# Kernel tuning notes

Measured on AMD Instinct MI355X. Metric: run time of the kernel, lower is better.

The kernel has to match this reference:

```python
import jax, jax.numpy as jnp
import numpy as np

B, D, T, H, CHUNK, MAX_REL = 4, 512, 8192, 8, 64, 2
HD = D // H


def setup_inputs() -> dict:
    key = jax.random.key(0)
    ks = jax.random.split(key, 16)
    s = 0.02
    inp = {
        "q": jax.random.normal(ks[0], (B, D, T), jnp.float32),
        "k": jax.random.normal(ks[1], (B, D, T), jnp.float32),
        "v": jax.random.normal(ks[2], (B, D, T), jnp.float32),
        "masks": jnp.ones((B, 1, T), jnp.float32),
        "Wq": jax.random.normal(ks[3], (D, D), jnp.float32) * s,
        "bq": jnp.zeros((D,), jnp.float32),
        "Wk": jax.random.normal(ks[4], (D, D), jnp.float32) * s,
        "bk": jnp.zeros((D,), jnp.float32),
        "Wv": jax.random.normal(ks[5], (D, D), jnp.float32) * s,
        "bv": jnp.zeros((D,), jnp.float32),
        "Wo": jax.random.normal(ks[6], (D, D), jnp.float32) * s,
        "bo": jnp.zeros((D,), jnp.float32),
        "rel_k": jax.random.normal(ks[7], (2 * MAX_REL + 1, HD), jnp.float32) * s,
        "rel_v": jax.random.normal(ks[8], (2 * MAX_REL + 1, HD), jnp.float32) * s,
    }
    return inp


def reference(q, k, v, masks, Wq, bq, Wk, bk, Wv, bv, Wo, bo, rel_k, rel_v):
    n = CHUNK
    g = T // n  # T is a multiple of chunck_size -> no padding branch
    bg = B * g

    # (B, D, T) -> (B, T, D) -> (B*g, n, D) chunking
    qt = jnp.swapaxes(q, 1, 2).reshape(bg, n, D)
    kt = jnp.swapaxes(k, 1, 2).reshape(bg, n, D)
    vt = jnp.swapaxes(v, 1, 2).reshape(bg, n, D)
    cm = jnp.swapaxes(masks, 1, 2).reshape(bg, n)  # per-chunk mask values

    # gen_key_padding_mask: chunks that are entirely zero are un-masked (set to 1)
    all_zero = jnp.sum(cm, axis=-1) == 0.0
    cm_fixed = jnp.where(all_zero[:, None], 1.0, cm)
    kpm = cm_fixed == 0.0  # (bg, n) True = masked key

    # projections (torch Linear: x @ W.T + b)
    qp = qt @ Wq.T + bq
    kp = kt @ Wk.T + bk
    vp = vt @ Wv.T + bv

    qh = qp.reshape(bg, n, H, HD).transpose(0, 2, 1, 3)  # (bg, H, n, hd)
    kh = kp.reshape(bg, n, H, HD).transpose(0, 2, 1, 3)
    vh = vp.reshape(bg, n, H, HD).transpose(0, 2, 1, 3)

    # content-content scores
    attn1 = jnp.einsum('bhqd,bhkd->bhqk', qh, kh)

    # relative position indices: clip(k - q, -max, max) + max
    ridx = jnp.clip(jnp.arange(n)[None, :] - jnp.arange(n)[:, None], -MAX_REL, MAX_REL) + MAX_REL
    rk = rel_k[ridx]  # (n, n, hd)
    rv = rel_v[ridx]  # (n, n, hd)

    # content-position scores
    attn2 = jnp.einsum('bhqd,qkd->bhqk', qh, rk)

    scale = jnp.sqrt(jnp.asarray(HD, jnp.float32))
    attn = (attn1 + attn2) / scale
    attn = jnp.where(kpm[:, None, None, :], -jnp.inf, attn)
    p = jax.nn.softmax(attn, axis=-1)  # (bg, H, n, n)

    w1 = jnp.einsum('bhqk,bhkd->bhqd', p, vh)
    w2 = jnp.einsum('bhqk,qkd->bhqd', p, rv)
    xo = (w1 + w2).transpose(0, 2, 1, 3).reshape(bg, n, D)
    xo = xo @ Wo.T + bo

    out = xo.reshape(B, T, D)
    out = jnp.swapaxes(out, 1, 2)  # (B, D, T)
    return out * masks
```

## Files before the change

### kernel.cpp

```cpp
#include <hip/hip_runtime.h>


typedef __attribute__((ext_vector_type(8))) short short8;
typedef __attribute__((ext_vector_type(4))) float f32x4;
typedef __attribute__((ext_vector_type(2))) unsigned int uint2v;
typedef __attribute__((ext_vector_type(4))) unsigned short ushort4v;

#define DEV static __device__ __forceinline__

DEV unsigned short f2bf(float f) {
  union { float f; unsigned int u; } x; x.f = f;
  unsigned int r = x.u + 0x7fffu + ((x.u >> 16) & 1u);
  return (unsigned short)(r >> 16);
}
DEV float bf2f(unsigned short h) {
  union { unsigned int u; float f; } x; x.u = ((unsigned int)h) << 16;
  return x.f;
}

constexpr int Bn = 4, Dm = 512, Tn = 8192, NC = 64;
constexpr int Gn = Tn / NC;
constexpr int BG = Bn * Gn;
constexpr int WSZ = Dm * Dm;

__global__ void wcvt_kernel(const float* __restrict__ wq, const float* __restrict__ wk,
                            const float* __restrict__ wv, const float* __restrict__ wo,
                            unsigned short* __restrict__ dst) {
  int i = (blockIdx.x * blockDim.x + threadIdx.x) * 4;
  const float* src = (i < WSZ) ? wq : (i < 2 * WSZ) ? wk : (i < 3 * WSZ) ? wv : wo;
  int off = i & (WSZ - 1);
  f32x4 v = *(const f32x4*)(src + off);
  ushort4v o;
  o[0] = f2bf(v[0]); o[1] = f2bf(v[1]); o[2] = f2bf(v[2]); o[3] = f2bf(v[3]);
  *(ushort4v*)(dst + i) = o;
}

__global__ __launch_bounds__(512, 2)
void fused_kernel(const float* __restrict__ qx, const float* __restrict__ kx,
                  const float* __restrict__ vx, const float* __restrict__ masks,
                  const unsigned short* __restrict__ wbf,
                  const float* __restrict__ bq, const float* __restrict__ bk,
                  const float* __restrict__ bv, const float* __restrict__ bo,
                  const float* __restrict__ relk, const float* __restrict__ relv,
                  float* __restrict__ out)
{
  extern __shared__ char lds[];
  const int tid  = threadIdx.x;
  const int lane = tid & 63;
  const int w    = tid >> 6;
  const int l15  = lane & 15;
  const int lg   = lane >> 4;
  const int c    = blockIdx.x;
  const int b    = c >> 7;
  const int t0   = (c & (Gn - 1)) * NC;

  char* xbuf = lds;
  char* regA = lds + 16 * 1024 + w * 16 * 1024;
  char* regB = regA + 8 * 1024;

  float cmv = masks[(size_t)b * Tn + t0 + lane];
  unsigned long long nzb = __ballot(cmv != 0.0f);
  unsigned long long kpm = (nzb == 0ull) ? 0ull : __ballot(cmv == 0.0f);

  const f32x4 fzero = {0.f, 0.f, 0.f, 0.f};

  auto project = [&](const float* __restrict__ xin, const unsigned short* __restrict__ Wp,
                     f32x4 (&acc)[4][4]) {
#pragma unroll
    for (int mi = 0; mi < 4; ++mi)
#pragma unroll
      for (int ni = 0; ni < 4; ++ni) acc[mi][ni] = fzero;
    const size_t xbase = (size_t)b * Dm * Tn + t0 + lane;
    for (int s = 0; s < 4; ++s) {
      const int d0 = s * 128;
      short8 xs[2];
#pragma unroll
      for (int cc = 0; cc < 2; ++cc)
#pragma unroll
        for (int j = 0; j < 8; ++j) {
          float f = xin[xbase + (size_t)(d0 + 16 * w + 8 * cc + j) * Tn];
          xs[cc][j] = (short)f2bf(f);
        }
      short8 wf[4][4];
#pragma unroll
      for (int ni = 0; ni < 4; ++ni)
#pragma unroll
        for (int kk = 0; kk < 4; ++kk) {
          int o = 64 * w + ni * 16 + l15;
          int d = d0 + kk * 32 + lg * 8;
          wf[ni][kk] = *(const short8*)(Wp + o * Dm + d);
        }
      __syncthreads();
#pragma unroll
      for (int cc = 0; cc < 2; ++cc) {
        int off = (lane * 256 + (16 * w + 8 * cc) * 2) ^ ((lane & 15) << 4);
        *(short8*)(xbuf + off) = xs[cc];
      }
      __syncthreads();
#pragma unroll
      for (int kk = 0; kk < 4; ++kk) {
        short8 af[4];
#pragma unroll
        for (int mi = 0; mi < 4; ++mi) {
          int t = mi * 16 + l15;
          int off = (t * 256 + (kk * 32 + lg * 8) * 2) ^ ((t & 15) << 4);
          af[mi] = *(const short8*)(xbuf + off);
        }
#pragma unroll
        for (int ni = 0; ni < 4; ++ni)
#pragma unroll
          for (int mi = 0; mi < 4; ++mi)
            acc[mi][ni] = __builtin_amdgcn_mfma_f32_16x16x32_bf16(af[mi], wf[ni][kk],
                                                                  acc[mi][ni], 0, 0, 0);
      }
    }
  };

  f32x4 acc[4][4];

  project(qx, wbf + 0 * WSZ, acc);
#pragma unroll
  for (int ni = 0; ni < 4; ++ni) {
    float bia = bq[64 * w + ni * 16 + l15];
    int hd = ni * 16 + l15;
#pragma unroll
    for (int mi = 0; mi < 4; ++mi)
#pragma unroll
      for (int rr = 0; rr < 4; ++rr) {
        int t = mi * 16 + lg * 4 + rr;
        int off = (t * 128 + hd * 2) ^ ((t & 7) << 4);
        *(unsigned short*)(regA + off) = f2bf(acc[mi][ni][rr] + bia);
      }
  }

  project(kx, wbf + 1 * WSZ, acc);
#pragma unroll
  for (int ni = 0; ni < 4; ++ni) {
    float bia = bk[64 * w + ni * 16 + l15];
    int hd = ni * 16 + l15;
#pragma unroll
    for (int mi = 0; mi < 4; ++mi)
#pragma unroll
      for (int rr = 0; rr < 4; ++rr) {
        int t = mi * 16 + lg * 4 + rr;
        int off = (t * 128 + hd * 2) ^ ((t & 7) << 4);
        *(unsigned short*)(regB + off) = f2bf(acc[mi][ni][rr] + bia);
      }
  }

  f32x4 sacc[4][4];
#pragma unroll
  for (int mi = 0; mi < 4; ++mi)
#pragma unroll
    for (int ni = 0; ni < 4; ++ni) sacc[mi][ni] = fzero;
#pragma unroll
  for (int kk = 0; kk < 2; ++kk) {
    short8 aq[4], bkf[4];
#pragma unroll
    for (int mi = 0; mi < 4; ++mi) {
      int t = mi * 16 + l15;
      int off = (t * 128 + (kk * 32 + lg * 8) * 2) ^ ((t & 7) << 4);
      aq[mi]  = *(const short8*)(regA + off);
      bkf[mi] = *(const short8*)(regB + off);
    }
#pragma unroll
    for (int ni = 0; ni < 4; ++ni)
#pragma unroll
      for (int mi = 0; mi < 4; ++mi)
        sacc[mi][ni] = __builtin_amdgcn_mfma_f32_16x16x32_bf16(aq[mi], bkf[ni],
                                                               sacc[mi][ni], 0, 0, 0);
  }

  float qr0 = 0, qr1 = 0, qr2 = 0, qr3 = 0, qr4 = 0;
#pragma unroll
  for (int g = 0; g < 8; ++g) {
    short8 q8 = *(const short8*)(regA + ((lane * 128 + g * 16) ^ ((lane & 7) << 4)));
#pragma unroll
    for (int j = 0; j < 8; ++j) {
      float qf = bf2f((unsigned short)q8[j]);
      qr0 += qf * relk[0 * 64 + g * 8 + j];
      qr1 += qf * relk[1 * 64 + g * 8 + j];
      qr2 += qf * relk[2 * 64 + g * 8 + j];
      qr3 += qf * relk[3 * 64 + g * 8 + j];
      qr4 += qf * relk[4 * 64 + g * 8 + j];
    }
  }

  const float scale = 0.125f;
#pragma unroll
  for (int mi = 0; mi < 4; ++mi)
#pragma unroll
    for (int rr = 0; rr < 4; ++rr) {
      int qt = mi * 16 + lg * 4 + rr;
      float q0 = __shfl(qr0, qt), q1 = __shfl(qr1, qt), q2 = __shfl(qr2, qt),
            q3 = __shfl(qr3, qt), q4 = __shfl(qr4, qt);
      float sv[4];
#pragma unroll
      for (int ni = 0; ni < 4; ++ni) {
        int kt = ni * 16 + l15;
        int dd = kt - qt;
        float a2 = (dd <= -2) ? q0 : (dd == -1) ? q1 : (dd == 0) ? q2 : (dd == 1) ? q3 : q4;
        float s = (sacc[mi][ni][rr] + a2) * scale;
        if ((kpm >> kt) & 1ull) s = -1e30f;
        sv[ni] = s;
      }
      float m = fmaxf(fmaxf(sv[0], sv[1]), fmaxf(sv[2], sv[3]));
#pragma unroll
      for (int xm = 1; xm < 16; xm <<= 1) m = fmaxf(m, __shfl_xor(m, xm));
      float ssum = 0.f;
#pragma unroll
      for (int ni = 0; ni < 4; ++ni) { sv[ni] = __expf(sv[ni] - m); ssum += sv[ni]; }
#pragma unroll
      for (int xm = 1; xm < 16; xm <<= 1) ssum += __shfl_xor(ssum, xm);
      float inv = 1.0f / ssum;
#pragma unroll
      for (int ni = 0; ni < 4; ++ni) {
        int kt = ni * 16 + l15;
        int off = (qt * 128 + kt * 2) ^ ((qt & 7) << 4);
        *(unsigned short*)(regB + off) = f2bf(sv[ni] * inv);
      }
    }

  float ps0 = 0, ps1 = 0, ps2 = 0, ps3 = 0, tot = 0;
#pragma unroll
  for (int g = 0; g < 8; ++g) {
    short8 p8 = *(const short8*)(regB + ((lane * 128 + g * 16) ^ ((lane & 7) << 4)));
#pragma unroll
    for (int j = 0; j < 8; ++j) {
      int kt = g * 8 + j;
      float p = bf2f((unsigned short)p8[j]);
      int dd = kt - lane;
      tot += p;
      ps0 += (dd <= -2) ? p : 0.f;
      ps1  = (dd == -1) ? p : ps1;
      ps2  = (dd ==  0) ? p : ps2;
      ps3  = (dd ==  1) ? p : ps3;
    }
  }
  float ps4 = tot - ps0 - ps1 - ps2 - ps3;

  project(vx, wbf + 2 * WSZ, acc);
#pragma unroll
  for (int ni = 0; ni < 4; ++ni) {
    float bia = bv[64 * w + ni * 16 + l15];
    int hd = ni * 16 + l15;
#pragma unroll
    for (int mi = 0; mi < 4; ++mi) {
      unsigned int lo = (unsigned int)f2bf(acc[mi][ni][0] + bia) |
                        ((unsigned int)f2bf(acc[mi][ni][1] + bia) << 16);
      unsigned int hi = (unsigned int)f2bf(acc[mi][ni][2] + bia) |
                        ((unsigned int)f2bf(acc[mi][ni][3] + bia) << 16);
      uint2v pk; pk[0] = lo; pk[1] = hi;
      int off = (hd * 128 + (mi * 16 + lg * 4) * 2) ^ ((hd & 7) << 4);
      *(uint2v*)(regA + off) = pk;
    }
  }

  f32x4 oacc[4][4];
#pragma unroll
  for (int mi = 0; mi < 4; ++mi)
#pragma unroll
    for (int ni = 0; ni < 4; ++ni) oacc[mi][ni] = fzero;
#pragma unroll
  for (int kk = 0; kk < 2; ++kk) {
    short8 av[4], bp[4];
#pragma unroll
    for (int mi = 0; mi < 4; ++mi) {
      int row = mi * 16 + l15;
      int off = (row * 128 + (kk * 32 + lg * 8) * 2) ^ ((row & 7) << 4);
      av[mi] = *(const short8*)(regA + off);
      bp[mi] = *(const short8*)(regB + off);
    }
#pragma unroll
    for (int ni = 0; ni < 4; ++ni)
#pragma unroll
      for (int mi = 0; mi < 4; ++mi)
        oacc[mi][ni] = __builtin_amdgcn_mfma_f32_16x16x32_bf16(av[mi], bp[ni],
                                                               oacc[mi][ni], 0, 0, 0);
  }

  float psh0[4], psh1[4], psh2[4], psh3[4], psh4[4];
#pragma unroll
  for (int ni = 0; ni < 4; ++ni) {
    int qt2 = ni * 16 + l15;
    psh0[ni] = __shfl(ps0, qt2); psh1[ni] = __shfl(ps1, qt2); psh2[ni] = __shfl(ps2, qt2);
    psh3[ni] = __shfl(ps3, qt2); psh4[ni] = __shfl(ps4, qt2);
  }
  uint2v xop[4][4];
#pragma unroll
  for (int mi = 0; mi < 4; ++mi) {
    float rv_[4][5];
#pragma unroll
    for (int rr = 0; rr < 4; ++rr) {
      int hd = mi * 16 + lg * 4 + rr;
#pragma unroll
      for (int r = 0; r < 5; ++r) rv_[rr][r] = relv[r * 64 + hd];
    }
#pragma unroll
    for (int ni = 0; ni < 4; ++ni) {
      unsigned short u[4];
#pragma unroll
      for (int rr = 0; rr < 4; ++rr) {
        float w2 = psh0[ni] * rv_[rr][0] + psh1[ni] * rv_[rr][1] + psh2[ni] * rv_[rr][2]
                 + psh3[ni] * rv_[rr][3] + psh4[ni] * rv_[rr][4];
        u[rr] = f2bf(oacc[mi][ni][rr] + w2);
      }
      uint2v pk; pk[0] = u[0] | ((unsigned int)u[1] << 16);
      pk[1] = u[2] | ((unsigned int)u[3] << 16);
      xop[mi][ni] = pk;
    }
  }

  __syncthreads();
  char* xobuf = lds + 16 * 1024;
#pragma unroll
  for (int ni = 0; ni < 4; ++ni) {
    int t = ni * 16 + l15;
#pragma unroll
    for (int mi = 0; mi < 4; ++mi) {
      int d = 64 * w + mi * 16 + lg * 4;
      int off = (t * 1024 + d * 2) ^ ((t & 15) << 4);
      *(uint2v*)(xobuf + off) = xop[mi][ni];
    }
  }
  __syncthreads();

  f32x4 cacc[4][4];
#pragma unroll
  for (int mi = 0; mi < 4; ++mi)
#pragma unroll
    for (int ni = 0; ni < 4; ++ni) cacc[mi][ni] = fzero;
  const unsigned short* Wo = wbf + 3 * WSZ;
#pragma unroll
  for (int kk = 0; kk < 16; ++kk) {
    short8 ax[4], bw[4];
#pragma unroll
    for (int mi = 0; mi < 4; ++mi) {
      int t = mi * 16 + l15;
      int off = (t * 1024 + (kk * 32 + lg * 8) * 2) ^ ((t & 15) << 4);
      ax[mi] = *(const short8*)(xobuf + off);
    }
#pragma unroll
    for (int ni = 0; ni < 4; ++ni) {
      int o = 64 * w + ni * 16 + l15;
      bw[ni] = *(const short8*)(Wo + o * Dm + kk * 32 + lg * 8);
    }
#pragma unroll
    for (int ni = 0; ni < 4; ++ni)
#pragma unroll
      for (int mi = 0; mi < 4; ++mi)
        cacc[mi][ni] = __builtin_amdgcn_mfma_f32_16x16x32_bf16(ax[mi], bw[ni],
                                                               cacc[mi][ni], 0, 0, 0);
  }
#pragma unroll
  for (int mi = 0; mi < 4; ++mi) {
    int tl = mi * 16 + lg * 4;
    f32x4 mv = *(const f32x4*)(masks + (size_t)b * Tn + t0 + tl);
#pragma unroll
    for (int ni = 0; ni < 4; ++ni) {
      int o = 64 * w + ni * 16 + l15;
      float bia = bo[o];
      f32x4 r;
#pragma unroll
      for (int rr = 0; rr < 4; ++rr) r[rr] = (cacc[mi][ni][rr] + bia) * mv[rr];
      *(f32x4*)(out + ((size_t)b * Dm + o) * Tn + t0 + tl) = r;
    }
  }
}

extern "C" void kernel_launch(void* const* d_in, const int* in_sizes, int n_in,
                              void* d_out, int out_size, void* d_ws, size_t ws_size,
                              hipStream_t stream) {
  (void)in_sizes; (void)n_in; (void)out_size; (void)ws_size;
  const float* q  = (const float*)d_in[0];
  const float* k  = (const float*)d_in[1];
  const float* v  = (const float*)d_in[2];
  const float* ms = (const float*)d_in[3];
  const float* Wq = (const float*)d_in[4];
  const float* bq = (const float*)d_in[5];
  const float* Wk = (const float*)d_in[6];
  const float* bk = (const float*)d_in[7];
  const float* Wv = (const float*)d_in[8];
  const float* bv = (const float*)d_in[9];
  const float* Wo = (const float*)d_in[10];
  const float* bo = (const float*)d_in[11];
  const float* rk = (const float*)d_in[12];
  const float* rv = (const float*)d_in[13];
  unsigned short* wbf = (unsigned short*)d_ws;
  float* out = (float*)d_out;

  wcvt_kernel<<<dim3(1024), dim3(256), 0, stream>>>(Wq, Wk, Wv, Wo, wbf);

  hipFuncSetAttribute((const void*)fused_kernel,
                      hipFuncAttributeMaxDynamicSharedMemorySize, 147456);
  fused_kernel<<<dim3(BG), dim3(512), 147456, stream>>>(q, k, v, ms, wbf,
                                                        bq, bk, bv, bo, rk, rv, out);
}
```

Baseline: 211.4 us.

## Pre-transpose inputs to bf16 tiled layout and feed fused kernel from global

Adds a pre-pass kernel that transposes q/k/v from (B,D,T) fp32 into a bf16 chunk-tiled layout in workspace, and retiles the bf16 weights so MFMA fragments load directly from global memory. A new fused kernel reads these pre-tiled operands without staging inputs through LDS, uses less shared memory, and computes the relative-position terms via per-row reductions. This trades an extra full read and write pass over the inputs for cheaper, contiguous operand loads in the main kernel. It falls back to the old path if the workspace is too small.

```diff
diff --git a/kernel.cpp b/kernel.cpp
--- a/kernel.cpp
+++ b/kernel.cpp
@@ -22,6 +22,357 @@
 constexpr int Gn = Tn / NC;
 constexpr int BG = Bn * Gn;
 constexpr int WSZ = Dm * Dm;
+constexpr size_t XTSZ = (size_t)Bn * Tn * Dm;
+
+__global__ __launch_bounds__(256) void wcvt_tiled(
+    const float* __restrict__ wq, const float* __restrict__ wk,
+    const float* __restrict__ wv, const float* __restrict__ wo,
+    unsigned short* __restrict__ dst) {
+  int i = blockIdx.x * 256 + threadIdx.x;
+  int m = i >> 16, fi = i & 65535;
+  int o = fi >> 7, d = (fi & 127) << 2;
+  const float* src = (m == 0) ? wq : (m == 1) ? wk : (m == 2) ? wv : wo;
+  f32x4 v = *(const f32x4*)(src + o * Dm + d);
+  ushort4v u;
+  u[0] = f2bf(v[0]); u[1] = f2bf(v[1]); u[2] = f2bf(v[2]); u[3] = f2bf(v[3]);
+  int doff = m * WSZ + ((o >> 6) << 15) + ((d >> 5) << 11) + ((o & 63) << 5) + (d & 31);
+  *(ushort4v*)(dst + doff) = u;
+}
+
+__global__ __launch_bounds__(256) void xpose_kernel(
+    const float* __restrict__ q, const float* __restrict__ k,
+    const float* __restrict__ v, unsigned short* __restrict__ xt) {
+  __shared__ unsigned short tile[64 * 65];
+  const int tid = threadIdx.x, bid = blockIdx.x;
+  const int tz = bid >> 12, rem = bid & 4095;
+  const int cid = rem >> 3, dh = rem & 7;
+  const int b = cid >> 7, t0 = (cid & 127) * 64, d0 = dh * 64;
+  const float* xin = (tz == 0) ? q : (tz == 1) ? k : v;
+  const int lane = tid & 63, drow = tid >> 6;
+  const size_t base = (size_t)b * Dm * Tn + t0 + lane;
+#pragma unroll
+  for (int p = 0; p < 16; ++p) {
+    int dr = drow + p * 4;
+    float f = xin[base + (size_t)(d0 + dr) * Tn];
+    tile[lane * 65 + dr] = f2bf(f);
+  }
+  __syncthreads();
+  unsigned short* xb = xt + (size_t)tz * XTSZ + ((size_t)cid << 15) + (dh << 12);
+  const int t = tid >> 2, dlo = (tid & 3) * 8;
+#pragma unroll
+  for (int h = 0; h < 2; ++h) {
+    short8 s;
+#pragma unroll
+    for (int j = 0; j < 8; ++j) s[j] = (short)tile[t * 65 + h * 32 + dlo + j];
+    *(short8*)(xb + h * 2048 + t * 32 + dlo) = s;
+  }
+}
+
+__global__ __launch_bounds__(512, 2)
+void fused2_kernel(const unsigned short* __restrict__ xt,
+                   const float* __restrict__ masks,
+                   const unsigned short* __restrict__ wbf,
+                   const float* __restrict__ bq, const float* __restrict__ bk,
+                   const float* __restrict__ bv, const float* __restrict__ bo,
+                   const float* __restrict__ relk, const float* __restrict__ relv,
+                   float* __restrict__ out)
+{
+  extern __shared__ char lds[];
+  const int tid  = threadIdx.x;
+  const int lane = tid & 63;
+  const int w    = tid >> 6;
+  const int l15  = lane & 15;
+  const int lg   = lane >> 4;
+  const int c    = blockIdx.x;
+  const int b    = c >> 7;
+  const int t0   = (c & (Gn - 1)) * NC;
+
+  char* regA = lds + w * 16384;
+  char* regB = regA + 8192;
+
+  float cmv = masks[(size_t)b * Tn + t0 + lane];
+  unsigned long long nzb = __ballot(cmv != 0.0f);
+  unsigned long long kpm = (nzb == 0ull) ? 0ull : __ballot(cmv == 0.0f);
+
+  const f32x4 fzero = {0.f, 0.f, 0.f, 0.f};
+  const int aoff = l15 * 32 + lg * 8;
+  const unsigned short* xq = xt + ((size_t)c << 15);
+  const unsigned short* xk = xq + XTSZ;
+  const unsigned short* xv = xq + 2 * XTSZ;
+
+  auto project = [&](const unsigned short* __restrict__ xb,
+                     const unsigned short* __restrict__ wb, f32x4 (&acc)[4][4]) {
+#pragma unroll
+    for (int mi = 0; mi < 4; ++mi)
+#pragma unroll
+      for (int ni = 0; ni < 4; ++ni) acc[mi][ni] = fzero;
+#pragma unroll
+    for (int kk = 0; kk < 16; ++kk) {
+      short8 af[4], bf_[4];
+#pragma unroll
+      for (int mi = 0; mi < 4; ++mi)
+        af[mi] = *(const short8*)(xb + kk * 2048 + mi * 512 + aoff);
+#pragma unroll
+      for (int ni = 0; ni < 4; ++ni)
+        bf_[ni] = *(const short8*)(wb + kk * 2048 + ni * 512 + aoff);
+#pragma unroll
+      for (int ni = 0; ni < 4; ++ni)
+#pragma unroll
+        for (int mi = 0; mi < 4; ++mi)
+          acc[mi][ni] = __builtin_amdgcn_mfma_f32_16x16x32_bf16(af[mi], bf_[ni],
+                                                                acc[mi][ni], 0, 0, 0);
+    }
+  };
+
+  f32x4 acc[4][4];
+
+  project(xq, wbf + 0 * WSZ + w * 32768, acc);
+#pragma unroll
+  for (int ni = 0; ni < 4; ++ni) {
+    float bia = bq[64 * w + ni * 16 + l15];
+    int hd = ni * 16 + l15;
+#pragma unroll
+    for (int mi = 0; mi < 4; ++mi)
+#pragma unroll
+      for (int rr = 0; rr < 4; ++rr) {
+        int t = mi * 16 + lg * 4 + rr;
+        int off = (t * 128 + hd * 2) ^ ((t & 7) << 4);
+        *(unsigned short*)(regA + off) = f2bf(acc[mi][ni][rr] + bia);
+      }
+  }
+
+  project(xk, wbf + 1 * WSZ + w * 32768, acc);
+#pragma unroll
+  for (int ni = 0; ni < 4; ++ni) {
+    float bia = bk[64 * w + ni * 16 + l15];
+    int hd = ni * 16 + l15;
+#pragma unroll
+    for (int mi = 0; mi < 4; ++mi)
+#pragma unroll
+      for (int rr = 0; rr < 4; ++rr) {
+        int t = mi * 16 + lg * 4 + rr;
+        int off = (t * 128 + hd * 2) ^ ((t & 7) << 4);
+        *(unsigned short*)(regB + off) = f2bf(acc[mi][ni][rr] + bia);
+      }
+  }
+
+  f32x4 sacc[4][4];
+#pragma unroll
+  for (int mi = 0; mi < 4; ++mi)
+#pragma unroll
+    for (int ni = 0; ni < 4; ++ni) sacc[mi][ni] = fzero;
+#pragma unroll
+  for (int kk = 0; kk < 2; ++kk) {
+    short8 aq[4], bkf[4];
+#pragma unroll
+    for (int mi = 0; mi < 4; ++mi) {
+      int t = mi * 16 + l15;
+      int off = (t * 128 + (kk * 32 + lg * 8) * 2) ^ ((t & 7) << 4);
+      aq[mi]  = *(const short8*)(regA + off);
+      bkf[mi] = *(const short8*)(regB + off);
+    }
+#pragma unroll
+    for (int ni = 0; ni < 4; ++ni)
+#pragma unroll
+      for (int mi = 0; mi < 4; ++mi)
+        sacc[mi][ni] = __builtin_amdgcn_mfma_f32_16x16x32_bf16(aq[mi], bkf[ni],
+                                                               sacc[mi][ni], 0, 0, 0);
+  }
+
+  float qr0 = 0, qr1 = 0, qr2 = 0, qr3 = 0, qr4 = 0;
+#pragma unroll
+  for (int g = 0; g < 8; ++g) {
+    short8 q8 = *(const short8*)(regA + ((lane * 128 + g * 16) ^ ((lane & 7) << 4)));
+#pragma unroll
+    for (int j = 0; j < 8; ++j) {
+      float qf = bf2f((unsigned short)q8[j]);
+      qr0 += qf * relk[0 * 64 + g * 8 + j];
+      qr1 += qf * relk[1 * 64 + g * 8 + j];
+      qr2 += qf * relk[2 * 64 + g * 8 + j];
+      qr3 += qf * relk[3 * 64 + g * 8 + j];
+      qr4 += qf * relk[4 * 64 + g * 8 + j];
+    }
+  }
+
+  const float scale = 0.125f;
+#pragma unroll
+  for (int mi = 0; mi < 4; ++mi)
+#pragma unroll
+    for (int rr = 0; rr < 4; ++rr) {
+      int qt = mi * 16 + lg * 4 + rr;
+      float q0 = __shfl(qr0, qt), q1 = __shfl(qr1, qt), q2 = __shfl(qr2, qt),
+            q3 = __shfl(qr3, qt), q4 = __shfl(qr4, qt);
+      float sv[4];
+#pragma unroll
+      for (int ni = 0; ni < 4; ++ni) {
+        int kt = ni * 16 + l15;
+        int dd = kt - qt;
+        float a2 = (dd <= -2) ? q0 : (dd == -1) ? q1 : (dd == 0) ? q2 : (dd == 1) ? q3 : q4;
+        float s = (sacc[mi][ni][rr] + a2) * scale;
+        if ((kpm >> kt) & 1ull) s = -1e30f;
+        sv[ni] = s;
+      }
+      float m = fmaxf(fmaxf(sv[0], sv[1]), fmaxf(sv[2], sv[3]));
+#pragma unroll
+      for (int xm = 1; xm < 16; xm <<= 1) m = fmaxf(m, __shfl_xor(m, xm));
+      float ssum = 0.f;
+#pragma unroll
+      for (int ni = 0; ni < 4; ++ni) { sv[ni] = __expf(sv[ni] - m); ssum += sv[ni]; }
+#pragma unroll
+      for (int xm = 1; xm < 16; xm <<= 1) ssum += __shfl_xor(ssum, xm);
+      float inv = 1.0f / ssum;
+#pragma unroll
+      for (int ni = 0; ni < 4; ++ni) {
+        int kt = ni * 16 + l15;
+        int off = (qt * 128 + kt * 2) ^ ((qt & 7) << 4);
+        *(unsigned short*)(regB + off) = f2bf(sv[ni] * inv);
+      }
+    }
+
+  float ps0 = 0, ps1 = 0, ps2 = 0, ps3 = 0, tot = 0;
+#pragma unroll
+  for (int g = 0; g < 8; ++g) {
+    short8 p8 = *(const short8*)(regB + ((lane * 128 + g * 16) ^ ((lane & 7) << 4)));
+#pragma unroll
+    for (int j = 0; j < 8; ++j) {
+      int kt = g * 8 + j;
+      float p = bf2f((unsigned short)p8[j]);
+      int dd = kt - lane;
+      tot += p;
+      ps0 += (dd <= -2) ? p : 0.f;
+      ps1  = (dd == -1) ? p : ps1;
+      ps2  = (dd ==  0) ? p : ps2;
+      ps3  = (dd ==  1) ? p : ps3;
+    }
+  }
+  float ps4 = tot - ps0 - ps1 - ps2 - ps3;
+
+  project(xv, wbf + 2 * WSZ + w * 32768, acc);
+#pragma unroll
+  for (int ni = 0; ni < 4; ++ni) {
+    float bia = bv[64 * w + ni * 16 + l15];
+    int hd = ni * 16 + l15;
+#pragma unroll
+    for (int mi = 0; mi < 4; ++mi) {
+      unsigned int lo = (unsigned int)f2bf(acc[mi][ni][0] + bia) |
+                        ((unsigned int)f2bf(acc[mi][ni][1] + bia) << 16);
+      unsigned int hi = (unsigned int)f2bf(acc[mi][ni][2] + bia) |
+                        ((unsigned int)f2bf(acc[mi][ni][3] + bia) << 16);
+      uint2v pk; pk[0] = lo; pk[1] = hi;
+      int off = (hd * 128 + (mi * 16 + lg * 4) * 2) ^ ((hd & 7) << 4);
+      *(uint2v*)(regA + off) = pk;
+    }
+  }
+
+  f32x4 oacc[4][4];
+#pragma unroll
+  for (int mi = 0; mi < 4; ++mi)
+#pragma unroll
+    for (int ni = 0; ni < 4; ++ni) oacc[mi][ni] = fzero;
+#pragma unroll
+  for (int kk = 0; kk < 2; ++kk) {
+    short8 av[4], bp[4];
+#pragma unroll
+    for (int mi = 0; mi < 4; ++mi) {
+      int row = mi * 16 + l15;
+      int off = (row * 128 + (kk * 32 + lg * 8) * 2) ^ ((row & 7) << 4);
+      av[mi] = *(const short8*)(regA + off);
+      bp[mi] = *(const short8*)(regB + off);
+    }
+#pragma unroll
+    for (int ni = 0; ni < 4; ++ni)
+#pragma unroll
+      for (int mi = 0; mi < 4; ++mi)
+        oacc[mi][ni] = __builtin_amdgcn_mfma_f32_16x16x32_bf16(av[mi], bp[ni],
+                                                               oacc[mi][ni], 0, 0, 0);
+  }
+
+  float psh0[4], psh1[4], psh2[4], psh3[4], psh4[4];
+#pragma unroll
+  for (int ni = 0; ni < 4; ++ni) {
+    int qt2 = ni * 16 + l15;
+    psh0[ni] = __shfl(ps0, qt2); psh1[ni] = __shfl(ps1, qt2); psh2[ni] = __shfl(ps2, qt2);
+    psh3[ni] = __shfl(ps3, qt2); psh4[ni] = __shfl(ps4, qt2);
+  }
+  uint2v xop[4][4];
+#pragma unroll
+  for (int mi = 0; mi < 4; ++mi) {
+    float rv_[4][5];
+#pragma unroll
+    for (int rr = 0; rr < 4; ++rr) {
+      int hd = mi * 16 + lg * 4 + rr;
+#pragma unroll
+      for (int r = 0; r < 5; ++r) rv_[rr][r] = relv[r * 64 + hd];
+    }
+#pragma unroll
+    for (int ni = 0; ni < 4; ++ni) {
+      unsigned short u[4];
+#pragma unroll
+      for (int rr = 0; rr < 4; ++rr) {
+        float w2 = psh0[ni] * rv_[rr][0] + psh1[ni] * rv_[rr][1] + psh2[ni] * rv_[rr][2]
+                 + psh3[ni] * rv_[rr][3] + psh4[ni] * rv_[rr][4];
+        u[rr] = f2bf(oacc[mi][ni][rr] + w2);
+      }
+      uint2v pk; pk[0] = u[0] | ((unsigned int)u[1] << 16);
+      pk[1] = u[2] | ((unsigned int)u[3] << 16);
+      xop[mi][ni] = pk;
+    }
+  }
+
+  __syncthreads();
+  char* xobuf = lds;
+#pragma unroll
+  for (int ni = 0; ni < 4; ++ni) {
+    int t = ni * 16 + l15;
+#pragma unroll
+    for (int mi = 0; mi < 4; ++mi) {
+      int d = 64 * w + mi * 16 + lg * 4;
+      int off = (t * 1024 + d * 2) ^ ((t & 15) << 4);
+      *(uint2v*)(xobuf + off) = xop[mi][ni];
+    }
+  }
+  __syncthreads();
+
+  f32x4 cacc[4][4];
+#pragma unroll
+  for (int mi = 0; mi < 4; ++mi)
+#pragma unroll
+    for (int ni = 0; ni < 4; ++ni) cacc[mi][ni] = fzero;
+  const unsigned short* wob = wbf + 3 * WSZ + w * 32768;
+#pragma unroll
+  for (int kk = 0; kk < 16; ++kk) {
+    short8 ax[4], bw[4];
+#pragma unroll
+    for (int mi = 0; mi < 4; ++mi) {
+      int t = mi * 16 + l15;
+      int off = (t * 1024 + (kk * 32 + lg * 8) * 2) ^ ((t & 15) << 4);
+      ax[mi] = *(const short8*)(xobuf + off);
+    }
+#pragma unroll
+    for (int ni = 0; ni < 4; ++ni)
+      bw[ni] = *(const short8*)(wob + kk * 2048 + ni * 512 + aoff);
+#pragma unroll
+    for (int ni = 0; ni < 4; ++ni)
+#pragma unroll
+      for (int mi = 0; mi < 4; ++mi)
+        cacc[mi][ni] = __builtin_amdgcn_mfma_f32_16x16x32_bf16(ax[mi], bw[ni],
+                                                               cacc[mi][ni], 0, 0, 0);
+  }
+#pragma unroll
+  for (int mi = 0; mi < 4; ++mi) {
+    int tl = mi * 16 + lg * 4;
+    f32x4 mv = *(const f32x4*)(masks + (size_t)b * Tn + t0 + tl);
+#pragma unroll
+    for (int ni = 0; ni < 4; ++ni) {
+      int o = 64 * w + ni * 16 + l15;
+      float bia = bo[o];
+      f32x4 r;
+#pragma unroll
+      for (int rr = 0; rr < 4; ++rr) r[rr] = (cacc[mi][ni][rr] + bia) * mv[rr];
+      *(f32x4*)(out + ((size_t)b * Dm + o) * Tn + t0 + tl) = r;
+    }
+  }
+}
 
 __global__ void wcvt_kernel(const float* __restrict__ wq, const float* __restrict__ wk,
                             const float* __restrict__ wv, const float* __restrict__ wo,
@@ -371,7 +722,7 @@
 extern "C" void kernel_launch(void* const* d_in, const int* in_sizes, int n_in,
                               void* d_out, int out_size, void* d_ws, size_t ws_size,
                               hipStream_t stream) {
-  (void)in_sizes; (void)n_in; (void)out_size; (void)ws_size;
+  (void)in_sizes; (void)n_in; (void)out_size;
   const float* q  = (const float*)d_in[0];
   const float* k  = (const float*)d_in[1];
   const float* v  = (const float*)d_in[2];
@@ -386,13 +737,24 @@
   const float* bo = (const float*)d_in[11];
   const float* rk = (const float*)d_in[12];
   const float* rv = (const float*)d_in[13];
+  float* out = (float*)d_out;
+
   unsigned short* wbf = (unsigned short*)d_ws;
-  float* out = (float*)d_out;
-
-  wcvt_kernel<<<dim3(1024), dim3(256), 0, stream>>>(Wq, Wk, Wv, Wo, wbf);
-
-  hipFuncSetAttribute((const void*)fused_kernel,
-                      hipFuncAttributeMaxDynamicSharedMemorySize, 147456);
-  fused_kernel<<<dim3(BG), dim3(512), 147456, stream>>>(q, k, v, ms, wbf,
-                                                        bq, bk, bv, bo, rk, rv, out);
+  const size_t need = (size_t)4 * WSZ * 2 + 3 * XTSZ * 2;
+
+  if (ws_size >= need) {
+    unsigned short* xt = wbf + 4 * WSZ;
+    wcvt_tiled<<<dim3(1024), dim3(256), 0, stream>>>(Wq, Wk, Wv, Wo, wbf);
+    xpose_kernel<<<dim3(12288), dim3(256), 0, stream>>>(q, k, v, xt);
+    hipFuncSetAttribute((const void*)fused2_kernel,
+                        hipFuncAttributeMaxDynamicSharedMemorySize, 131072);
+    fused2_kernel<<<dim3(BG), dim3(512), 131072, stream>>>(xt, ms, wbf,
+                                                           bq, bk, bv, bo, rk, rv, out);
+  } else {
+    wcvt_kernel<<<dim3(1024), dim3(256), 0, stream>>>(Wq, Wk, Wv, Wo, wbf);
+    hipFuncSetAttribute((const void*)fused_kernel,
+                        hipFuncAttributeMaxDynamicSharedMemorySize, 147456);
+    fused_kernel<<<dim3(BG), dim3(512), 147456, stream>>>(q, k, v, ms, wbf,
+                                                          bq, bk, bv, bo, rk, rv, out);
+  }
 }
```

After: 210.6 us. About the same (-0.3%).
